# Performance work log

Measured on AMD Instinct MI355X. Metric: run time of the kernel, lower is better.

The kernel has to match this reference:

```python
import jax, jax.numpy as jnp
import numpy as np

EMBED_DIM = 512
BATCH = 4
SEQ = 4096

def setup_inputs() -> dict:
    key = jax.random.key(0)
    k1, k2, k3, k4 = jax.random.split(key, 4)
    inputs = jax.random.normal(k1, (BATCH, SEQ, EMBED_DIM), dtype=jnp.float32)
    scale = 1.0 / np.sqrt(EMBED_DIM)
    Wq = jax.random.normal(k2, (EMBED_DIM, EMBED_DIM), dtype=jnp.float32) * scale
    Wk = jax.random.normal(k3, (EMBED_DIM, EMBED_DIM), dtype=jnp.float32) * scale
    Wv = jax.random.normal(k4, (EMBED_DIM, EMBED_DIM), dtype=jnp.float32) * scale
    temperature = jnp.float32(1.0)
    return {"inputs": inputs, "Wq": Wq, "Wk": Wk, "Wv": Wv, "temperature": temperature}

def reference(inputs, Wq, Wk, Wv, temperature):
    # nn.Linear with weight W computes x @ W.T; we store W as (out,in)-equivalent square,
    # applied as x @ W.T for faithfulness.
    Q = jnp.einsum('bsd,ed->bse', inputs, Wq)
    K = jnp.einsum('bsd,ed->bse', inputs, Wk)
    V = jnp.einsum('bsd,ed->bse', inputs, Wv)
    d = inputs.shape[-1]
    scores = jnp.einsum('bqe,bke->bqk', Q, K) * (temperature / jnp.sqrt(jnp.float32(d)))  # [B,S,S]
    attn = jax.nn.softmax(scores, axis=-1)
    return jnp.einsum('bqk,bke->bqe', attn, V)
```

## Files before the change

kernel.cpp:

```cpp
#include <hip/hip_runtime.h>
#include <hip/hip_bf16.h>
#include <stdint.h>

typedef __bf16 bf16;
typedef bf16 bf16x8 __attribute__((ext_vector_type(8)));
typedef bf16 bf16x4 __attribute__((ext_vector_type(4)));
typedef float f32x4 __attribute__((ext_vector_type(4)));

#define MFMA16(a, b, c) __builtin_amdgcn_mfma_f32_16x16x32_bf16((a), (b), (c), 0, 0, 0)

__device__ __forceinline__ void async_ld16(bf16* lds, const bf16* g) {
    __builtin_amdgcn_global_load_lds(
        (const __attribute__((address_space(1))) void*)g,
        (__attribute__((address_space(3))) void*)lds, 16, 0, 0);
}

__global__ __launch_bounds__(256) void proj_kernel(
    const float* __restrict__ X,
    const float* __restrict__ Wq,
    const float* __restrict__ Wk,
    const float* __restrict__ Wv,
    bf16* __restrict__ Qo,
    bf16* __restrict__ Ko,
    bf16* __restrict__ Vt)
{
    __shared__ bf16 As[128][72];
    __shared__ bf16 Bs[128][72];

    const int z    = blockIdx.z;
    const float* W = (z == 0) ? Wq : (z == 1) ? Wk : Wv;
    const int row0 = blockIdx.x * 128;
    const int col0 = blockIdx.y * 128;

    const int t    = threadIdx.x;
    const int w    = t >> 6;
    const int lane = t & 63;
    const int lg   = lane >> 4;
    const int lc   = lane & 15;
    const int wr   = (w >> 1) * 64;
    const int wc   = (w & 1) * 64;

    const int srow = t >> 1;
    const int sd0  = (t & 1) * 16;

    f32x4 acc[4][4];
    for (int a = 0; a < 4; ++a)
        for (int b = 0; b < 4; ++b)
            acc[a][b] = (f32x4){0.f, 0.f, 0.f, 0.f};

    for (int kt = 0; kt < 16; ++kt) {
        const int k = kt * 32;
        __syncthreads();
        {
            const float* xs = X + (size_t)(row0 + srow) * 512 + k + sd0;
            float4 a0 = *(const float4*)(xs + 0);
            float4 a1 = *(const float4*)(xs + 4);
            float4 a2 = *(const float4*)(xs + 8);
            float4 a3 = *(const float4*)(xs + 12);
            bf16x8 h0 = { (bf16)a0.x, (bf16)a0.y, (bf16)a0.z, (bf16)a0.w,
                          (bf16)a1.x, (bf16)a1.y, (bf16)a1.z, (bf16)a1.w };
            bf16x8 h1 = { (bf16)a2.x, (bf16)a2.y, (bf16)a2.z, (bf16)a2.w,
                          (bf16)a3.x, (bf16)a3.y, (bf16)a3.z, (bf16)a3.w };
            *(bf16x8*)&As[srow][sd0]     = h0;
            *(bf16x8*)&As[srow][sd0 + 8] = h1;

            const float* ws_ = W + (size_t)(col0 + srow) * 512 + k + sd0;
            float4 b0 = *(const float4*)(ws_ + 0);
            float4 b1 = *(const float4*)(ws_ + 4);
            float4 b2 = *(const float4*)(ws_ + 8);
            float4 b3 = *(const float4*)(ws_ + 12);
            bf16x8 g0 = { (bf16)b0.x, (bf16)b0.y, (bf16)b0.z, (bf16)b0.w,
                          (bf16)b1.x, (bf16)b1.y, (bf16)b1.z, (bf16)b1.w };
            bf16x8 g1 = { (bf16)b2.x, (bf16)b2.y, (bf16)b2.z, (bf16)b2.w,
                          (bf16)b3.x, (bf16)b3.y, (bf16)b3.z, (bf16)b3.w };
            *(bf16x8*)&Bs[srow][sd0]     = g0;
            *(bf16x8*)&Bs[srow][sd0 + 8] = g1;
        }
        __syncthreads();

        bf16x8 af[4], bfr[4];
        for (int fr = 0; fr < 4; ++fr)
            af[fr] = *(const bf16x8*)&As[wr + fr * 16 + lc][lg * 8];
        for (int fc = 0; fc < 4; ++fc)
            bfr[fc] = *(const bf16x8*)&Bs[wc + fc * 16 + lc][lg * 8];
        for (int fr = 0; fr < 4; ++fr)
            for (int fc = 0; fc < 4; ++fc)
                acc[fr][fc] = MFMA16(af[fr], bfr[fc], acc[fr][fc]);
    }

    if (z < 2) {
        bf16* outp = (z == 0) ? Qo : Ko;
        for (int fr = 0; fr < 4; ++fr)
            for (int fc = 0; fc < 4; ++fc) {
                const int colg = col0 + wc + fc * 16 + lc;
                const int rowb = row0 + wr + fr * 16 + lg * 4;
                for (int i = 0; i < 4; ++i)
                    outp[(size_t)(rowb + i) * 512 + colg] = (bf16)acc[fr][fc][i];
            }
    } else {
        for (int fr = 0; fr < 4; ++fr)
            for (int fc = 0; fc < 4; ++fc) {
                const int e    = col0 + wc + fc * 16 + lc;
                const int rowb = row0 + wr + fr * 16 + lg * 4;
                const int bb   = rowb >> 12;
                const int sl   = rowb & 4095;
                bf16x4 v = { (bf16)acc[fr][fc][0], (bf16)acc[fr][fc][1],
                             (bf16)acc[fr][fc][2], (bf16)acc[fr][fc][3] };
                *(bf16x4*)&Vt[(((size_t)(bb * 512 + e)) << 12) + sl] = v;
            }
    }
}

__global__ __launch_bounds__(512) void flash_kernel(
    const bf16* __restrict__ Q,
    const bf16* __restrict__ K,
    const bf16* __restrict__ Vt,
    const float* __restrict__ temp,
    float* __restrict__ Out)
{
    extern __shared__ char smem[];
    bf16* Kb = (bf16*)smem;
    bf16* Pb = (bf16*)(smem + 2 * 64 * 512 * 2);
    __shared__ float l_part[64][2];

    const int L  = blockIdx.x;
    const int b  = (L & 7) >> 1;
    const int q0 = (((L & 1) << 5) + (L >> 3)) << 6;

    const int t    = threadIdx.x;
    const int w    = t >> 6;
    const int lane = t & 63;
    const int lg   = lane >> 4;
    const int lc   = lane & 15;
    const int qrb  = (w >> 1) * 16;
    const int par  = w & 1;

    const float scale2 = temp[0] * 0.04419417382415922f * 1.4426950408889634f;

    const bf16* kbase = K  + (size_t)b * 4096 * 512;
    const bf16* vbase = Vt + (size_t)b * 512 * 4096;

#pragma unroll
    for (int j = 0; j < 8; ++j) {
        const int r = w * 8 + j;
        async_ld16(Kb + (size_t)r * 512,
                   kbase + (size_t)r * 512 + ((lane ^ j) << 3));
    }

    bf16x8 qf[16];
    {
        const bf16* qrow = Q + ((size_t)(b * 4096 + q0 + qrb + lc)) * 512 + lg * 8;
#pragma unroll
        for (int kt = 0; kt < 16; ++kt)
            qf[kt] = *(const bf16x8*)(qrow + kt * 32);
    }

    f32x4 acc[4][4];
    for (int a = 0; a < 4; ++a)
        for (int c = 0; c < 4; ++c)
            acc[a][c] = (f32x4){0.f, 0.f, 0.f, 0.f};
    float Lacc[4] = {0.f, 0.f, 0.f, 0.f};

    __syncthreads();

    const int r7  = lc & 7;
    const int xlo = (lg ^ (r7 & 3)) << 3;
    const int xb2 = (r7 & 4) << 3;

    for (int it = 0; it < 64; ++it) {
        const int cur = it & 1;
        const bf16* Kc = Kb + (size_t)cur * 32768;

        const bf16* vb0 = vbase + (size_t)(w * 64 + lc) * 4096 + it * 64 + lg * 8;
        bf16x8 vv[8];
#pragma unroll
        for (int kk2 = 0; kk2 < 2; ++kk2)
#pragma unroll
            for (int fc = 0; fc < 4; ++fc)
                vv[kk2 * 4 + fc] =
                    *(const bf16x8*)(vb0 + (size_t)fc * 16 * 4096 + kk2 * 32);

        {
            const int nxt = (it + 1) & 63;
            bf16* Kn = Kb + (size_t)(cur ^ 1) * 32768;
            const bf16* knx = kbase + (size_t)nxt * 64 * 512;
#pragma unroll
            for (int j = 0; j < 8; ++j) {
                const int r = w * 8 + j;
                async_ld16(Kn + (size_t)r * 512,
                           knx + (size_t)r * 512 + ((lane ^ j) << 3));
            }
        }

        asm volatile("s_waitcnt vmcnt(16)" ::: "memory");
        __builtin_amdgcn_s_barrier();

        f32x4 s0 = (f32x4){0.f, 0.f, 0.f, 0.f};
        f32x4 s1 = (f32x4){0.f, 0.f, 0.f, 0.f};
        const bf16* kr0 = Kc + (size_t)(par * 32 + lc) * 512 + xlo;
        const bf16* kr1 = kr0 + (size_t)16 * 512;
#pragma unroll
        for (int kt = 0; kt < 16; ++kt) {
            const int off = (kt * 32) ^ xb2;
            bf16x8 k0 = *(const bf16x8*)(kr0 + off);
            bf16x8 k1 = *(const bf16x8*)(kr1 + off);
            s0 = MFMA16(qf[kt], k0, s0);
            s1 = MFMA16(qf[kt], k1, s1);
        }

#pragma unroll
        for (int i = 0; i < 4; ++i) {
            const int row = qrb + lg * 4 + i;
            float p0 = __builtin_amdgcn_exp2f(s0[i] * scale2);
            float p1 = __builtin_amdgcn_exp2f(s1[i] * scale2);
            Pb[row * 72 + par * 32 + lc]      = (bf16)p0;
            Pb[row * 72 + par * 32 + 16 + lc] = (bf16)p1;
            Lacc[i] += p0 + p1;
        }

        asm volatile("s_waitcnt lgkmcnt(0)" ::: "memory");
        __builtin_amdgcn_s_barrier();

#pragma unroll
        for (int kk2 = 0; kk2 < 2; ++kk2) {
            bf16x8 pa[4];
#pragma unroll
            for (int fr = 0; fr < 4; ++fr)
                pa[fr] = *(const bf16x8*)&Pb[(fr * 16 + lc) * 72 + kk2 * 32 + lg * 8];
#pragma unroll
            for (int fc = 0; fc < 4; ++fc)
#pragma unroll
                for (int fr = 0; fr < 4; ++fr)
                    acc[fr][fc] = MFMA16(pa[fr], vv[kk2 * 4 + fc], acc[fr][fc]);
        }
    }

#pragma unroll
    for (int d = 1; d < 16; d <<= 1)
#pragma unroll
        for (int i = 0; i < 4; ++i)
            Lacc[i] += __shfl_xor(Lacc[i], d);
    if (lc == 0)
#pragma unroll
        for (int i = 0; i < 4; ++i)
            l_part[qrb + lg * 4 + i][par] = Lacc[i];
    __syncthreads();

    for (int fr = 0; fr < 4; ++fr) {
        float invl[4];
#pragma unroll
        for (int i = 0; i < 4; ++i) {
            const int row = fr * 16 + lg * 4 + i;
            invl[i] = 1.0f / (l_part[row][0] + l_part[row][1]);
        }
        for (int fc = 0; fc < 4; ++fc) {
            const size_t base =
                ((size_t)(b * 4096 + q0 + fr * 16 + lg * 4)) * 512 + w * 64 + fc * 16 + lc;
#pragma unroll
            for (int i = 0; i < 4; ++i)
                Out[base + (size_t)i * 512] = acc[fr][fc][i] * invl[i];
        }
    }
}

extern "C" void kernel_launch(void* const* d_in, const int* in_sizes, int n_in,
                              void* d_out, int out_size, void* d_ws, size_t ws_size,
                              hipStream_t stream) {
    const float* X    = (const float*)d_in[0];
    const float* Wq   = (const float*)d_in[1];
    const float* Wk   = (const float*)d_in[2];
    const float* Wv   = (const float*)d_in[3];
    const float* temp = (const float*)d_in[4];
    float* Out = (float*)d_out;

    const size_t NE = (size_t)4 * 4096 * 512;
    bf16* Qw = (bf16*)d_ws;
    bf16* Kw = Qw + NE;
    bf16* Vt = Kw + NE;

    proj_kernel<<<dim3(128, 4, 3), 256, 0, stream>>>(X, Wq, Wk, Wv, Qw, Kw, Vt);

    const size_t smem_bytes = (size_t)2 * 64 * 512 * 2 + (size_t)64 * 72 * 2;
    flash_kernel<<<dim3(256), 512, smem_bytes, stream>>>(Qw, Kw, Vt, temp, Out);
}
```

Before: 308.2 us.

## Split KV range across two blocks, single-buffer K, add combine kernel

Templates the flash kernel with a split-KV mode in which each query tile is handled by two blocks covering half of the key sequence each. This doubles the grid from 256 to 512 blocks so more CUs are busy. Each half writes unnormalized partial outputs and row sums, and a new combine kernel adds them and normalizes. K staging is cut from double to single buffering, with an extra barrier before the next tile's load, which halves LDS use to allow more resident blocks. The cost is an extra fp32 output round trip through memory, one more launch, and less overlap of K loads with compute.

```diff
diff --git a/kernel.cpp b/kernel.cpp
--- a/kernel.cpp
+++ b/kernel.cpp
@@ -111,21 +111,34 @@
     }
 }
 
-__global__ __launch_bounds__(512) void flash_kernel(
+template<bool SPLIT>
+__global__ __launch_bounds__(512, 4) void flash_kernel(
     const bf16* __restrict__ Q,
     const bf16* __restrict__ K,
     const bf16* __restrict__ Vt,
     const float* __restrict__ temp,
-    float* __restrict__ Out)
+    float* __restrict__ Out,
+    float* __restrict__ O1,
+    float* __restrict__ lsum)
 {
     extern __shared__ char smem[];
     bf16* Kb = (bf16*)smem;
-    bf16* Pb = (bf16*)(smem + 2 * 64 * 512 * 2);
+    bf16* Pb = (bf16*)(smem + 64 * 512 * 2);
     __shared__ float l_part[64][2];
 
-    const int L  = blockIdx.x;
-    const int b  = (L & 7) >> 1;
-    const int q0 = (((L & 1) << 5) + (L >> 3)) << 6;
+    const int L = blockIdx.x;
+    int b, q0, z;
+    if (SPLIT) {
+        z  = L & 1;
+        b  = (L >> 1) & 3;
+        q0 = (L >> 3) << 6;
+    } else {
+        z  = 0;
+        b  = (L & 7) >> 1;
+        q0 = (((L & 1) << 5) + (L >> 3)) << 6;
+    }
+    const int NIT   = SPLIT ? 32 : 64;
+    const int kvoff = SPLIT ? z * 2048 : 0;
 
     const int t    = threadIdx.x;
     const int w    = t >> 6;
@@ -137,8 +150,8 @@
 
     const float scale2 = temp[0] * 0.04419417382415922f * 1.4426950408889634f;
 
-    const bf16* kbase = K  + (size_t)b * 4096 * 512;
-    const bf16* vbase = Vt + (size_t)b * 512 * 4096;
+    const bf16* kbase = K  + (size_t)(b * 4096 + kvoff) * 512;
+    const bf16* vbase = Vt + (size_t)b * 512 * 4096 + kvoff;
 
 #pragma unroll
     for (int j = 0; j < 8; ++j) {
@@ -167,10 +180,7 @@
     const int xlo = (lg ^ (r7 & 3)) << 3;
     const int xb2 = (r7 & 4) << 3;
 
-    for (int it = 0; it < 64; ++it) {
-        const int cur = it & 1;
-        const bf16* Kc = Kb + (size_t)cur * 32768;
-
+    for (int it = 0; it < NIT; ++it) {
         const bf16* vb0 = vbase + (size_t)(w * 64 + lc) * 4096 + it * 64 + lg * 8;
         bf16x8 vv[8];
 #pragma unroll
@@ -180,24 +190,12 @@
                 vv[kk2 * 4 + fc] =
                     *(const bf16x8*)(vb0 + (size_t)fc * 16 * 4096 + kk2 * 32);
 
-        {
-            const int nxt = (it + 1) & 63;
-            bf16* Kn = Kb + (size_t)(cur ^ 1) * 32768;
-            const bf16* knx = kbase + (size_t)nxt * 64 * 512;
-#pragma unroll
-            for (int j = 0; j < 8; ++j) {
-                const int r = w * 8 + j;
-                async_ld16(Kn + (size_t)r * 512,
-                           knx + (size_t)r * 512 + ((lane ^ j) << 3));
-            }
-        }
-
-        asm volatile("s_waitcnt vmcnt(16)" ::: "memory");
+        asm volatile("s_waitcnt vmcnt(8)" ::: "memory");
         __builtin_amdgcn_s_barrier();
 
         f32x4 s0 = (f32x4){0.f, 0.f, 0.f, 0.f};
         f32x4 s1 = (f32x4){0.f, 0.f, 0.f, 0.f};
-        const bf16* kr0 = Kc + (size_t)(par * 32 + lc) * 512 + xlo;
+        const bf16* kr0 = Kb + (size_t)(par * 32 + lc) * 512 + xlo;
         const bf16* kr1 = kr0 + (size_t)16 * 512;
 #pragma unroll
         for (int kt = 0; kt < 16; ++kt) {
@@ -206,6 +204,19 @@
             bf16x8 k1 = *(const bf16x8*)(kr1 + off);
             s0 = MFMA16(qf[kt], k0, s0);
             s1 = MFMA16(qf[kt], k1, s1);
+        }
+
+        __builtin_amdgcn_s_barrier();
+
+        {
+            const int nxt = (it + 1) & (NIT - 1);
+            const bf16* knx = kbase + (size_t)nxt * 64 * 512;
+#pragma unroll
+            for (int j = 0; j < 8; ++j) {
+                const int r = w * 8 + j;
+                async_ld16(Kb + (size_t)r * 512,
+                           knx + (size_t)r * 512 + ((lane ^ j) << 3));
+            }
         }
 
 #pragma unroll
@@ -246,21 +257,56 @@
             l_part[qrb + lg * 4 + i][par] = Lacc[i];
     __syncthreads();
 
-    for (int fr = 0; fr < 4; ++fr) {
-        float invl[4];
-#pragma unroll
-        for (int i = 0; i < 4; ++i) {
-            const int row = fr * 16 + lg * 4 + i;
-            invl[i] = 1.0f / (l_part[row][0] + l_part[row][1]);
-        }
-        for (int fc = 0; fc < 4; ++fc) {
-            const size_t base =
-                ((size_t)(b * 4096 + q0 + fr * 16 + lg * 4)) * 512 + w * 64 + fc * 16 + lc;
-#pragma unroll
-            for (int i = 0; i < 4; ++i)
-                Out[base + (size_t)i * 512] = acc[fr][fc][i] * invl[i];
-        }
-    }
+    if (SPLIT) {
+        float* Og = (z == 0) ? Out : O1;
+        if (t < 64)
+            lsum[(size_t)(z * 4 + b) * 4096 + q0 + t] =
+                l_part[t][0] + l_part[t][1];
+        for (int fr = 0; fr < 4; ++fr)
+            for (int fc = 0; fc < 4; ++fc) {
+                const size_t base =
+                    ((size_t)(b * 4096 + q0 + fr * 16 + lg * 4)) * 512 +
+                    w * 64 + fc * 16 + lc;
+#pragma unroll
+                for (int i = 0; i < 4; ++i)
+                    Og[base + (size_t)i * 512] = acc[fr][fc][i];
+            }
+    } else {
+        for (int fr = 0; fr < 4; ++fr) {
+            float invl[4];
+#pragma unroll
+            for (int i = 0; i < 4; ++i) {
+                const int row = fr * 16 + lg * 4 + i;
+                invl[i] = 1.0f / (l_part[row][0] + l_part[row][1]);
+            }
+            for (int fc = 0; fc < 4; ++fc) {
+                const size_t base =
+                    ((size_t)(b * 4096 + q0 + fr * 16 + lg * 4)) * 512 +
+                    w * 64 + fc * 16 + lc;
+#pragma unroll
+                for (int i = 0; i < 4; ++i)
+                    Out[base + (size_t)i * 512] = acc[fr][fc][i] * invl[i];
+            }
+        }
+    }
+}
+
+__global__ __launch_bounds__(256) void combine_kernel(
+    float* __restrict__ Out,
+    const float* __restrict__ O1,
+    const float* __restrict__ lsum)
+{
+    const int idx = blockIdx.x * 256 + threadIdx.x;
+    const int row = idx >> 7;
+    float4 a = ((const float4*)Out)[idx];
+    float4 c = ((const float4*)O1)[idx];
+    const float inv = 1.0f / (lsum[row] + lsum[16384 + row]);
+    float4 r;
+    r.x = (a.x + c.x) * inv;
+    r.y = (a.y + c.y) * inv;
+    r.z = (a.z + c.z) * inv;
+    r.w = (a.w + c.w) * inv;
+    ((float4*)Out)[idx] = r;
 }
 
 extern "C" void kernel_launch(void* const* d_in, const int* in_sizes, int n_in,
@@ -277,9 +323,20 @@
     bf16* Qw = (bf16*)d_ws;
     bf16* Kw = Qw + NE;
     bf16* Vt = Kw + NE;
+    float* O1   = (float*)(Vt + NE);
+    float* lsum = O1 + NE;
 
     proj_kernel<<<dim3(128, 4, 3), 256, 0, stream>>>(X, Wq, Wk, Wv, Qw, Kw, Vt);
 
-    const size_t smem_bytes = (size_t)2 * 64 * 512 * 2 + (size_t)64 * 72 * 2;
-    flash_kernel<<<dim3(256), 512, smem_bytes, stream>>>(Qw, Kw, Vt, temp, Out);
-}
+    const size_t smem_bytes = (size_t)64 * 512 * 2 + (size_t)64 * 72 * 2;
+    const size_t ws_needed  = 3 * NE * 2 + NE * 4 + (size_t)2 * 4 * 4096 * 4;
+
+    if (ws_size >= ws_needed) {
+        flash_kernel<true><<<dim3(512), 512, smem_bytes, stream>>>(
+            Qw, Kw, Vt, temp, Out, O1, lsum);
+        combine_kernel<<<dim3(8192), 256, 0, stream>>>(Out, O1, lsum);
+    } else {
+        flash_kernel<false><<<dim3(256), 512, smem_bytes, stream>>>(
+            Qw, Kw, Vt, temp, Out, nullptr, nullptr);
+    }
+}
```

Result: slower. 867.2 us (+181.4%).

## Software-pipeline QK^T of tile i with PV of tile i-1 using double-buffered P

Applied to the files above, without the earlier changes.

Restructures the flash attention loop so the P·V MFMAs for the previous key tile are interleaved with the Q·K^T MFMAs for the current tile. P is double-buffered in LDS and V registers alternate between two sets. This removes one barrier per iteration and lets the matrix units work on independent chains while exp and LDS traffic proceed. The cost is more registers (a second V set), twice the LDS for P, and a manually unrolled prologue and epilogue.

```diff
diff --git a/kernel.cpp b/kernel.cpp
--- a/kernel.cpp
+++ b/kernel.cpp
@@ -161,79 +161,118 @@
             acc[a][c] = (f32x4){0.f, 0.f, 0.f, 0.f};
     float Lacc[4] = {0.f, 0.f, 0.f, 0.f};
 
+    bf16x8 vvA[8], vvB[8];
+
     __syncthreads();
 
     const int r7  = lc & 7;
     const int xlo = (lg ^ (r7 & 3)) << 3;
     const int xb2 = (r7 & 4) << 3;
 
-    for (int it = 0; it < 64; ++it) {
-        const int cur = it & 1;
-        const bf16* Kc = Kb + (size_t)cur * 32768;
-
-        const bf16* vb0 = vbase + (size_t)(w * 64 + lc) * 4096 + it * 64 + lg * 8;
-        bf16x8 vv[8];
-#pragma unroll
-        for (int kk2 = 0; kk2 < 2; ++kk2)
-#pragma unroll
-            for (int fc = 0; fc < 4; ++fc)
-                vv[kk2 * 4 + fc] =
-                    *(const bf16x8*)(vb0 + (size_t)fc * 16 * 4096 + kk2 * 32);
-
-        {
-            const int nxt = (it + 1) & 63;
-            bf16* Kn = Kb + (size_t)(cur ^ 1) * 32768;
-            const bf16* knx = kbase + (size_t)nxt * 64 * 512;
-#pragma unroll
-            for (int j = 0; j < 8; ++j) {
-                const int r = w * 8 + j;
-                async_ld16(Kn + (size_t)r * 512,
-                           knx + (size_t)r * 512 + ((lane ^ j) << 3));
-            }
-        }
-
-        asm volatile("s_waitcnt vmcnt(16)" ::: "memory");
-        __builtin_amdgcn_s_barrier();
-
-        f32x4 s0 = (f32x4){0.f, 0.f, 0.f, 0.f};
-        f32x4 s1 = (f32x4){0.f, 0.f, 0.f, 0.f};
-        const bf16* kr0 = Kc + (size_t)(par * 32 + lc) * 512 + xlo;
-        const bf16* kr1 = kr0 + (size_t)16 * 512;
-#pragma unroll
-        for (int kt = 0; kt < 16; ++kt) {
-            const int off = (kt * 32) ^ xb2;
-            bf16x8 k0 = *(const bf16x8*)(kr0 + off);
-            bf16x8 k1 = *(const bf16x8*)(kr1 + off);
-            s0 = MFMA16(qf[kt], k0, s0);
-            s1 = MFMA16(qf[kt], k1, s1);
-        }
-
-#pragma unroll
-        for (int i = 0; i < 4; ++i) {
-            const int row = qrb + lg * 4 + i;
-            float p0 = __builtin_amdgcn_exp2f(s0[i] * scale2);
-            float p1 = __builtin_amdgcn_exp2f(s1[i] * scale2);
-            Pb[row * 72 + par * 32 + lc]      = (bf16)p0;
-            Pb[row * 72 + par * 32 + 16 + lc] = (bf16)p1;
-            Lacc[i] += p0 + p1;
-        }
-
-        asm volatile("s_waitcnt lgkmcnt(0)" ::: "memory");
-        __builtin_amdgcn_s_barrier();
-
+#define ITER_BODY(IT, KC, vvLD, vvPV, DO_PV, DO_PF)                            \
+    {                                                                          \
+                             \
+        if (DO_PF) {                                                           \
+            bf16* Kn = Kb + (size_t)((KC) ^ 1) * 32768;                        \
+            const bf16* knx = kbase + (size_t)((IT) + 1) * 64 * 512;           \
+            _Pragma("unroll")                                                  \
+            for (int j = 0; j < 8; ++j) {                                      \
+                const int r = w * 8 + j;                                       \
+                async_ld16(Kn + (size_t)r * 512,                               \
+                           knx + (size_t)r * 512 + ((lane ^ j) << 3));         \
+            }                                                                  \
+        }                                                                      \
+                          \
+        {                                                                      \
+            const bf16* vb0 = vbase + (size_t)(w * 64 + lc) * 4096             \
+                              + (IT) * 64 + lg * 8;                            \
+            _Pragma("unroll")                                                  \
+            for (int kk2 = 0; kk2 < 2; ++kk2)                                  \
+                _Pragma("unroll")                                              \
+                for (int fc = 0; fc < 4; ++fc)                                 \
+                    vvLD[kk2 * 4 + fc] = *(const bf16x8*)(                     \
+                        vb0 + (size_t)fc * 16 * 4096 + kk2 * 32);              \
+        }                                                                      \
+             \
+        f32x4 s0 = (f32x4){0.f, 0.f, 0.f, 0.f};                                \
+        f32x4 s1 = (f32x4){0.f, 0.f, 0.f, 0.f};                                \
+        {                                                                      \
+            const bf16* Kc  = Kb + (size_t)(KC) * 32768;                       \
+            const bf16* Pp  = Pb + (size_t)((KC) ^ 1) * (64 * 72);             \
+            const bf16* kr0 = Kc + (size_t)(par * 32 + lc) * 512 + xlo;        \
+            const bf16* kr1 = kr0 + (size_t)16 * 512;                          \
+            _Pragma("unroll")                                                  \
+            for (int half = 0; half < 2; ++half) {                             \
+                bf16x8 pa[4];                                                  \
+                if (DO_PV) {                                                   \
+                    _Pragma("unroll")                                          \
+                    for (int fr = 0; fr < 4; ++fr)                             \
+                        pa[fr] = *(const bf16x8*)&Pp[(fr * 16 + lc) * 72       \
+                                                     + half * 32 + lg * 8];    \
+                }                                                              \
+                _Pragma("unroll")                                              \
+                for (int kh = 0; kh < 8; ++kh) {                               \
+                    const int kt  = half * 8 + kh;                             \
+                    const int off = (kt * 32) ^ xb2;                           \
+                    bf16x8 k0 = *(const bf16x8*)(kr0 + off);                   \
+                    bf16x8 k1 = *(const bf16x8*)(kr1 + off);                   \
+                    s0 = MFMA16(qf[kt], k0, s0);                               \
+                    s1 = MFMA16(qf[kt], k1, s1);                               \
+                    if (DO_PV) {                                               \
+                        const int fc = kh >> 1;                                \
+                        const int f0 = (kh & 1) * 2;                           \
+                        acc[f0][fc]     = MFMA16(pa[f0],                       \
+                            vvPV[half * 4 + fc], acc[f0][fc]);                 \
+                        acc[f0 + 1][fc] = MFMA16(pa[f0 + 1],                   \
+                            vvPV[half * 4 + fc], acc[f0 + 1][fc]);             \
+                    }                                                          \
+                }                                                              \
+            }                                                                  \
+        }                                                                      \
+                              \
+        {                                                                      \
+            bf16* Pc = Pb + (size_t)(KC) * (64 * 72);                          \
+            _Pragma("unroll")                                                  \
+            for (int i = 0; i < 4; ++i) {                                      \
+                const int row = qrb + lg * 4 + i;                              \
+                float p0 = __builtin_amdgcn_exp2f(s0[i] * scale2);             \
+                float p1 = __builtin_amdgcn_exp2f(s1[i] * scale2);             \
+                Pc[row * 72 + par * 32 + lc]      = (bf16)p0;                  \
+                Pc[row * 72 + par * 32 + 16 + lc] = (bf16)p1;                  \
+                Lacc[i] += p0 + p1;                                            \
+            }                                                                  \
+        }                                                                      \
+              \
+        asm volatile("s_waitcnt vmcnt(8) lgkmcnt(0)" ::: "memory");            \
+        __builtin_amdgcn_s_barrier();                                          \
+    }
+
+    ITER_BODY(0, 0, vvA, vvB, false, true)
+
+    for (int t2 = 0; t2 < 31; ++t2) {
+        const int i = 2 * t2 + 1;
+        ITER_BODY(i,     1, vvB, vvA, true, true)
+        ITER_BODY(i + 1, 0, vvA, vvB, true, true)
+    }
+
+    ITER_BODY(63, 1, vvB, vvA, true, false)
+
+    {
+        const bf16* Pp = Pb + (size_t)1 * (64 * 72);
 #pragma unroll
         for (int kk2 = 0; kk2 < 2; ++kk2) {
             bf16x8 pa[4];
 #pragma unroll
             for (int fr = 0; fr < 4; ++fr)
-                pa[fr] = *(const bf16x8*)&Pb[(fr * 16 + lc) * 72 + kk2 * 32 + lg * 8];
+                pa[fr] = *(const bf16x8*)&Pp[(fr * 16 + lc) * 72 + kk2 * 32 + lg * 8];
 #pragma unroll
             for (int fc = 0; fc < 4; ++fc)
 #pragma unroll
                 for (int fr = 0; fr < 4; ++fr)
-                    acc[fr][fc] = MFMA16(pa[fr], vv[kk2 * 4 + fc], acc[fr][fc]);
+                    acc[fr][fc] = MFMA16(pa[fr], vvB[kk2 * 4 + fc], acc[fr][fc]);
         }
     }
+#undef ITER_BODY
 
 #pragma unroll
     for (int d = 1; d < 16; d <<= 1)
@@ -280,6 +319,6 @@
 
     proj_kernel<<<dim3(128, 4, 3), 256, 0, stream>>>(X, Wq, Wk, Wv, Qw, Kw, Vt);
 
-    const size_t smem_bytes = (size_t)2 * 64 * 512 * 2 + (size_t)64 * 72 * 2;
+    const size_t smem_bytes = (size_t)2 * 64 * 512 * 2 + (size_t)2 * 64 * 72 * 2;
     flash_kernel<<<dim3(256), 512, smem_bytes, stream>>>(Qw, Kw, Vt, temp, Out);
 }
```

Measured after the change: 288.2 us. 6.5% less time.
